# Kernel tuning notes

Hardware: AMD Instinct MI355X
Metric: run time of the kernel (lower is better)

The kernel has to match this reference:

```python
import jax, jax.numpy as jnp
import numpy as np

# NVFP4 E2M1 representable magnitudes and decision midpoints (round-to-nearest)
_E2M1_GRID = np.array([0.0, 0.5, 1.0, 1.5, 2.0, 3.0, 4.0, 6.0], dtype=np.float32)
_E2M1_MIDS = np.array([0.25, 0.75, 1.25, 1.75, 2.5, 3.5, 5.0], dtype=np.float32)
_BLOCK = 16  # quant_tile_shape=(1,16)


def fake_quant_nvfp4(t):
    """Blockwise (16 contiguous elems) E2M1 fake quant with pow2 scales."""
    shape = t.shape
    v = t.reshape(-1, _BLOCK)                      # [n_blocks, 16]
    amax = jnp.max(jnp.abs(v), axis=-1, keepdims=True)
    # power-of-2 scale so that amax/scale <= 6 (E2M1 max)
    exp = jnp.ceil(jnp.log2(jnp.maximum(amax, jnp.float32(1e-30)) / 6.0))
    scale = jnp.where(amax > 0, jnp.exp2(exp), jnp.float32(1.0))
    u = v / scale
    a = jnp.abs(u)
    grid = jnp.asarray(_E2M1_GRID, dtype=t.dtype)
    mids = jnp.asarray(_E2M1_MIDS, dtype=t.dtype)
    idx = jnp.digitize(a, mids)                    # nearest E2M1 magnitude index
    q = jnp.sign(u) * grid[idx]
    return (q * scale).reshape(shape)


def setup_inputs() -> dict:
    key = jax.random.key(0)
    kx, kw = jax.random.split(key)
    x = jax.random.normal(kx, (32, 256, 64, 64), dtype=jnp.float32)
    w = jax.random.normal(kw, (256, 256, 3, 3), dtype=jnp.float32) * 0.05
    return {"x": x, "w": w}


def reference(x, w):
    qx = fake_quant_nvfp4(x)
    qw = fake_quant_nvfp4(w)
    # conv2d, stride 1, padding 1, no bias, NCHW / OIHW
    return jax.lax.conv_general_dilated(
        qx, qw,
        window_strides=(1, 1),
        padding=((1, 1), (1, 1)),
        dimension_numbers=("NCHW", "OIHW", "NCHW"),
    )
```

## Files before the change

kernel.cpp:

```cpp
#include <hip/hip_runtime.h>
#include <stdint.h>
#include <stddef.h>

typedef __attribute__((ext_vector_type(8))) short short8;
typedef __attribute__((ext_vector_type(4))) float f32x4;

#define N_IMG 32
#define C_IN  256
#define HH    64
#define WW    64
#define O_OUT 256
#define HP    66
#define WP    66

#define QX_ELEMS (N_IMG*HP*WP*C_IN)
#define QX_BYTES ((size_t)QX_ELEMS*2)
#define QW_ELEMS (9*O_OUT*C_IN)


__device__ __forceinline__ float e2m1_mag(float a) {
    return a < 0.25f ? 0.0f
         : a < 0.75f ? 0.5f
         : a < 1.25f ? 1.0f
         : a < 1.75f ? 1.5f
         : a < 2.5f  ? 2.0f
         : a < 3.5f  ? 3.0f
         : a < 5.0f  ? 4.0f : 6.0f;
}

__device__ __forceinline__ void blk_scale2(float amax, float& s, float& inv) {
    float ac = fmaxf(amax, 1e-30f);
    int e;
    float m = frexpf(ac, &e);
    int ex = (m > 0.75f) ? (e - 2) : (e - 3);
    if (amax > 0.0f) { s = ldexpf(1.0f, ex); inv = ldexpf(1.0f, -ex); }
    else             { s = 1.0f; inv = 1.0f; }
}

__device__ __forceinline__ unsigned short to_bf16_bits(float v) {
    union { float f; unsigned int u; } cv; cv.f = v;
    return (unsigned short)(cv.u >> 16);
}

__global__ __launch_bounds__(256) void halo_zero_kernel(unsigned short* __restrict__ qx) {
    int id = blockIdx.x * 256 + threadIdx.x;
    size_t off;
    if (id < 135168) {
        int n = id / 4224, r = id % 4224;
        int h = (r / 2112) * 65;
        int k = r % 2112;
        off = (((size_t)(n*HP + h)) * WP) * C_IN + (size_t)k * 8;
    } else {
        int j = id - 135168;
        int n = j >> 12, r = j & 4095;
        int h = 1 + (r >> 6);
        int w = ((r >> 5) & 1) * 65;
        int k = r & 31;
        off = (((size_t)(n*HP + h)) * WP + w) * C_IN + (size_t)k * 8;
    }
    uint4 z; z.x = z.y = z.z = z.w = 0u;
    *(uint4*)(qx + off) = z;
}

__global__ __launch_bounds__(256) void quant_x_kernel(const float* __restrict__ x,
                                                      unsigned short* __restrict__ qx) {
    __shared__ float xf[64][65];
    __shared__ float sarr[4][65];
    __shared__ float iarr[4][65];

    const int bid = blockIdx.x;
    const int n  = bid >> 8;
    const int h  = (bid >> 2) & 63;
    const int cb = bid & 3;
    const int t  = threadIdx.x;

    {
        const int rb = t >> 4;
        const int w4 = (t & 15) * 4;
        const float* src = x + (((size_t)(n*C_IN + cb*64)) * HH + h) * WW;
#pragma unroll
        for (int it = 0; it < 4; ++it) {
            int r = it * 16 + rb;
            float4 g = *(const float4*)(src + (size_t)r * (HH*WW) + w4);
            xf[r][w4+0] = g.x; xf[r][w4+1] = g.y; xf[r][w4+2] = g.z; xf[r][w4+3] = g.w;
        }
    }
    __syncthreads();

    {
        const int c = t >> 2, wb = t & 3;
        float amax = 0.f;
#pragma unroll
        for (int j = 0; j < 16; ++j) amax = fmaxf(amax, fabsf(xf[c][wb*16 + j]));
        float s, inv;
        blk_scale2(amax, s, inv);
        sarr[wb][c] = s;
        iarr[wb][c] = inv;
    }
    __syncthreads();

    {
        const int w = t >> 2, cg = (t & 3) * 16, wb = w >> 4;
        unsigned short outv[16];
#pragma unroll
        for (int i = 0; i < 16; ++i) {
            int c = cg + i;
            float v = xf[c][w];
            float q = copysignf(e2m1_mag(fabsf(v) * iarr[wb][c]) * sarr[wb][c], v);
            outv[i] = to_bf16_bits(q);
        }
        unsigned short* dst = qx + (((size_t)(n*HP + h + 1)) * WP + (w + 1)) * C_IN + cb*64 + cg;
        *(uint4*)(dst)     = *(const uint4*)&outv[0];
        *(uint4*)(dst + 8) = *(const uint4*)&outv[8];
    }
}

__global__ __launch_bounds__(256) void quant_w_kernel(const float* __restrict__ w,
                                                      unsigned short* __restrict__ qw) {
    __shared__ unsigned short lq[2304];
    const int o = blockIdx.x;
    const int t = threadIdx.x;
    const float* src = w + (size_t)o * 2304;
    if (t < 144) {
        float v[16];
#pragma unroll
        for (int j = 0; j < 4; ++j) {
            float4 f = ((const float4*)(src + t*16))[j];
            v[j*4+0]=f.x; v[j*4+1]=f.y; v[j*4+2]=f.z; v[j*4+3]=f.w;
        }
        float amax = 0.f;
#pragma unroll
        for (int j = 0; j < 16; ++j) amax = fmaxf(amax, fabsf(v[j]));
        float s, inv;
        blk_scale2(amax, s, inv);
#pragma unroll
        for (int j = 0; j < 16; ++j)
            lq[t*16 + j] = to_bf16_bits(copysignf(e2m1_mag(fabsf(v[j]) * inv) * s, v[j]));
    }
    __syncthreads();
#pragma unroll
    for (int p = 0; p < 9; ++p)
        qw[((size_t)(p*O_OUT + o)) * C_IN + t] = lq[t*9 + p];
}

__device__ __forceinline__ void gld16(void* lds, const void* g) {
    __builtin_amdgcn_global_load_lds(
        (const __attribute__((address_space(1))) unsigned int*)g,
        (__attribute__((address_space(3))) unsigned int*)lds,
        16, 0, 0);
}

__device__ __forceinline__ short8 rd8(const void* p) {
    return *(const short8*)p;
}

#define MFMA16 __builtin_amdgcn_mfma_f32_16x16x32_bf16

#define MM16(I0, A00, A01, A10, A11)                                      \
    do {                                                                  \
        _Pragma("unroll")                                                 \
        for (int j = 0; j < 4; ++j) {                                     \
            acc[I0][j]     = MFMA16(A00, b[j][0], acc[I0][j],     0,0,0); \
            acc[I0][j]     = MFMA16(A01, b[j][1], acc[I0][j],     0,0,0); \
            acc[(I0)+1][j] = MFMA16(A10, b[j][0], acc[(I0)+1][j], 0,0,0); \
            acc[(I0)+1][j] = MFMA16(A11, b[j][1], acc[(I0)+1][j], 0,0,0); \
        }                                                                 \
    } while (0)

#define PHASE(Q, S1, S2, VM)                                              \
    do {                                                                  \
        short8 aa0 = rd8(LA + rA + (2*(Q))*2048   + cA0);                 \
        short8 aa1 = rd8(LA + rA + (2*(Q))*2048   + (cA0^64));            \
        short8 aa2 = rd8(LA + rA + (2*(Q)+1)*2048 + cA0);                 \
        short8 aa3 = rd8(LA + rA + (2*(Q)+1)*2048 + (cA0^64));            \
        S1; S2;                                                           \
        __builtin_amdgcn_s_barrier();                                     \
        asm volatile("s_waitcnt lgkmcnt(0)" ::: "memory");                \
        __builtin_amdgcn_sched_barrier(0);                                \
        __builtin_amdgcn_s_setprio(1);                                    \
        MM16(2*(Q), aa0, aa1, aa2, aa3);                                  \
        __builtin_amdgcn_s_setprio(0);                                    \
        asm volatile("s_waitcnt " VM ::: "memory");                       \
        __builtin_amdgcn_s_barrier();                                     \
    } while (0)

__global__ __launch_bounds__(512) void conv_kernel(const unsigned short* __restrict__ qw,
                                                   const unsigned short* __restrict__ qx,
                                                   float* __restrict__ out) {
    __shared__ unsigned short lds[65536];
    char* Lc = (char*)lds;

    const int tid  = threadIdx.x;
    const int w    = tid >> 6;
    const int lane = tid & 63;
    const int lo16 = lane & 15;
    const int quad = lane >> 4;
    const int wm   = w & 1;
    const int wn   = w >> 1;

    const int id  = blockIdx.x;
    const int idx = id >> 3;
    const int n   = (id & 7) + ((idx >> 4) << 3);
    const int pt  = idx & 15;
    const int h0  = pt * 4;
    const int hw0 = pt * 256;

    const int trow  = tid >> 3;
    const int c_off = ((tid & 7) ^ (trow & 7)) << 3;
    const unsigned short* gB = qx + ((size_t)((n*HP + h0 + 1) * WP + trow + 1)) * C_IN + c_off;
    const int ro0 = trow + ((tid >= 256) ? 96 : 0);
    const unsigned short* gA = qw + (size_t)ro0 * C_IN + c_off;
    const int awb = w * 1024 + ((w < 4) ? 0 : 12288);
    const int bwb = w * 1024;

    const int key = (lo16 & 7) << 4;
    const int cA0 = (quad << 4) ^ key;
    const int rA  = (wm * 128 + lo16) * 128;
    const int rB  = (wn * 64  + lo16) * 128;

    f32x4 acc[8][4];
#pragma unroll
    for (int i = 0; i < 8; ++i)
#pragma unroll
        for (int j = 0; j < 4; ++j)
            acc[i][j] = (f32x4){0.f, 0.f, 0.f, 0.f};

    {
        const unsigned short* ga = gA;
        const unsigned short* gb = gB - 17152;
        char* SA = Lc;
        char* SB = Lc + 32768;
        gld16(SB + bwb,         gb);
        gld16(SB + bwb + 8192,  gb + 16896);
        gld16(SB + bwb + 16384, gb + 2*16896);
        gld16(SB + bwb + 24576, gb + 3*16896);
        gld16(SA + awb,         ga);
        gld16(SA + awb + 4096,  ga + 8192);
        gld16(SA + awb + 8192,  ga + 16384);
        gld16(SA + awb + 12288, ga + 24576);
        asm volatile("s_waitcnt vmcnt(0)" ::: "memory");
        __builtin_amdgcn_s_barrier();
    }

    int curOff = 0;
#pragma unroll 1
    for (int t = 0; t < 36; ++t) {
        const int tn  = (t < 35) ? (t + 1) : 35;
        const int pn  = tn >> 2;
        const int qn  = pn / 3;
        const int dwn = pn - qn * 3;
        const int cn  = (tn & 3) << 6;
        const unsigned short* ga = gA + pn * 65536 + cn;
        const unsigned short* gb = gB + (ptrdiff_t)((qn - 1) * WP + (dwn - 1)) * C_IN + cn;

        const char* LA = Lc + curOff;
        const char* LB = LA + 32768;
        char* SA = Lc + (curOff ^ 65536);
        char* SB = SA + 32768;

        short8 b[4][2];
#pragma unroll
        for (int j = 0; j < 4; ++j) {
            b[j][0] = rd8(LB + rB + j*2048 + cA0);
            b[j][1] = rd8(LB + rB + j*2048 + (cA0^64));
        }

        PHASE(0, gld16(SB + bwb,         gb),
                 gld16(SB + bwb + 8192,  gb + 16896),   "vmcnt(4)");
        PHASE(1, gld16(SB + bwb + 16384, gb + 2*16896),
                 gld16(SB + bwb + 24576, gb + 3*16896), "vmcnt(5)");
        PHASE(2, gld16(SA + awb,         ga),
                 gld16(SA + awb + 4096,  ga + 8192),    "vmcnt(6)");
        PHASE(3, gld16(SA + awb + 8192,  ga + 16384),
                 gld16(SA + awb + 12288, ga + 24576),   "vmcnt(3)");

        curOff ^= 65536;
    }

#pragma unroll
    for (int i = 0; i < 8; ++i) {
        const int o = wm * 128 + i * 16 + quad * 4;
        float* orow = out + ((size_t)(n * O_OUT + o)) * (HH*WW) + hw0 + wn * 64 + lo16;
#pragma unroll
        for (int j = 0; j < 4; ++j) {
            float* dst = orow + j * 16;
#pragma unroll
            for (int r = 0; r < 4; ++r)
                dst[(size_t)r * (HH*WW)] = acc[i][j][r];
        }
    }
}

extern "C" void kernel_launch(void* const* d_in, const int* in_sizes, int n_in,
                              void* d_out, int out_size, void* d_ws, size_t ws_size,
                              hipStream_t stream) {
    const float* x = (const float*)d_in[0];
    const float* w = (const float*)d_in[1];
    float* out = (float*)d_out;

    unsigned short* qx = (unsigned short*)d_ws;
    unsigned short* qw = (unsigned short*)((char*)d_ws + QX_BYTES);

    halo_zero_kernel<<<dim3(1040), 256, 0, stream>>>(qx);
    quant_x_kernel<<<dim3(N_IMG*HH*4), 256, 0, stream>>>(x, qx);
    quant_w_kernel<<<dim3(O_OUT), 256, 0, stream>>>(w, qw);
    conv_kernel<<<dim3(512), 512, 0, stream>>>(qw, qx, out);
}
```

Baseline: 363.3 us.

## Software-pipeline LDS fragment reads one phase ahead of MFMA in conv main loop

Restructures the main loop so each phase issues the LDS reads for the next A-fragment group before running the current MFMAs. The B fragments for the next tile are read during the last phase, using ping-pong registers. The loop is unrolled by two to alternate buffers, and the vmcnt wait counts are adjusted to match. This hides LDS read latency behind matrix work, at the cost of more live registers (roughly double the A/B fragment registers) and tighter waitcnt correctness requirements.

```diff
diff --git a/kernel.cpp b/kernel.cpp
--- a/kernel.cpp
+++ b/kernel.cpp
@@ -156,32 +156,81 @@
 
 #define MFMA16 __builtin_amdgcn_mfma_f32_16x16x32_bf16
 
-#define MM16(I0, A00, A01, A10, A11)                                      \
+#define MM16(I0, A00, A01, A10, A11, B)                                   \
     do {                                                                  \
         _Pragma("unroll")                                                 \
         for (int j = 0; j < 4; ++j) {                                     \
-            acc[I0][j]     = MFMA16(A00, b[j][0], acc[I0][j],     0,0,0); \
-            acc[I0][j]     = MFMA16(A01, b[j][1], acc[I0][j],     0,0,0); \
-            acc[(I0)+1][j] = MFMA16(A10, b[j][0], acc[(I0)+1][j], 0,0,0); \
-            acc[(I0)+1][j] = MFMA16(A11, b[j][1], acc[(I0)+1][j], 0,0,0); \
+            acc[I0][j]     = MFMA16(A00, B[j][0], acc[I0][j],     0,0,0); \
+            acc[I0][j]     = MFMA16(A01, B[j][1], acc[I0][j],     0,0,0); \
+            acc[(I0)+1][j] = MFMA16(A10, B[j][0], acc[(I0)+1][j], 0,0,0); \
+            acc[(I0)+1][j] = MFMA16(A11, B[j][1], acc[(I0)+1][j], 0,0,0); \
         }                                                                 \
     } while (0)
 
-#define PHASE(Q, S1, S2, VM)                                              \
+#define RDQ(D0, D1, D2, D3, Q)                                            \
+    D0 = rd8(LA + rA + (2*(Q))*2048   + cA0);                             \
+    D1 = rd8(LA + rA + (2*(Q))*2048   + (cA0^64));                        \
+    D2 = rd8(LA + rA + (2*(Q)+1)*2048 + cA0);                             \
+    D3 = rd8(LA + rA + (2*(Q)+1)*2048 + (cA0^64));
+
+#define PH_OPEN()                                                         \
+    __builtin_amdgcn_s_barrier();                                         \
+    asm volatile("s_waitcnt lgkmcnt(0)" ::: "memory");                    \
+    __builtin_amdgcn_sched_barrier(0);                                    \
+    __builtin_amdgcn_s_setprio(1);
+
+#define PH_CLOSE(VM)                                                      \
+    __builtin_amdgcn_s_setprio(0);                                        \
+    asm volatile("s_waitcnt " VM ::: "memory");                           \
+    __builtin_amdgcn_s_barrier();
+
+#define CONV_TILE(TN, LAOFF, BCUR, BNXT)                                  \
     do {                                                                  \
-        short8 aa0 = rd8(LA + rA + (2*(Q))*2048   + cA0);                 \
-        short8 aa1 = rd8(LA + rA + (2*(Q))*2048   + (cA0^64));            \
-        short8 aa2 = rd8(LA + rA + (2*(Q)+1)*2048 + cA0);                 \
-        short8 aa3 = rd8(LA + rA + (2*(Q)+1)*2048 + (cA0^64));            \
-        S1; S2;                                                           \
-        __builtin_amdgcn_s_barrier();                                     \
-        asm volatile("s_waitcnt lgkmcnt(0)" ::: "memory");                \
-        __builtin_amdgcn_sched_barrier(0);                                \
-        __builtin_amdgcn_s_setprio(1);                                    \
-        MM16(2*(Q), aa0, aa1, aa2, aa3);                                  \
-        __builtin_amdgcn_s_setprio(0);                                    \
-        asm volatile("s_waitcnt " VM ::: "memory");                       \
-        __builtin_amdgcn_s_barrier();                                     \
+        const int tn  = (TN);                                             \
+        const int pn  = tn >> 2;                                          \
+        const int qn  = pn / 3;                                           \
+        const int dwn = pn - qn * 3;                                      \
+        const int cn  = (tn & 3) << 6;                                    \
+        const unsigned short* ga = gA + pn * 65536 + cn;                  \
+        const unsigned short* gb = gB + (ptrdiff_t)((qn - 1) * WP + (dwn - 1)) * C_IN + cn; \
+        const char* LA = Lc + (LAOFF);                                    \
+        char* SA = Lc + ((LAOFF) ^ 65536);                                \
+        char* SB = SA + 32768;                                            \
+        short8 aA0, aA1, aA2, aA3, aB0, aB1, aB2, aB3;                    \
+        \
+        RDQ(aA0, aA1, aA2, aA3, 0);                                       \
+                     \
+        gld16(SB + bwb,        gb);                                       \
+        gld16(SB + bwb + 8192, gb + 16896);                               \
+        PH_OPEN();                                                        \
+        RDQ(aB0, aB1, aB2, aB3, 1);                                       \
+        MM16(0, aA0, aA1, aA2, aA3, BCUR);                                \
+        PH_CLOSE("vmcnt(3)");                                             \
+                            \
+        gld16(SB + bwb + 16384, gb + 2*16896);                            \
+        gld16(SB + bwb + 24576, gb + 3*16896);                            \
+        PH_OPEN();                                                        \
+        RDQ(aA0, aA1, aA2, aA3, 2);                                       \
+        MM16(2, aB0, aB1, aB2, aB3, BCUR);                                \
+        PH_CLOSE("vmcnt(4)");                                             \
+                            \
+        gld16(SA + awb,        ga);                                       \
+        gld16(SA + awb + 4096, ga + 8192);                                \
+        PH_OPEN();                                                        \
+        RDQ(aB0, aB1, aB2, aB3, 3);                                       \
+        MM16(4, aA0, aA1, aA2, aA3, BCUR);                                \
+        PH_CLOSE("vmcnt(2)");                                             \
+          \
+        gld16(SA + awb + 8192,  ga + 16384);                              \
+        gld16(SA + awb + 12288, ga + 24576);                              \
+        PH_OPEN();                                                        \
+        _Pragma("unroll")                                                 \
+        for (int j = 0; j < 4; ++j) {                                     \
+            BNXT[j][0] = rd8(SB + rB + j*2048 + cA0);                     \
+            BNXT[j][1] = rd8(SB + rB + j*2048 + (cA0^64));                \
+        }                                                                 \
+        MM16(6, aB0, aB1, aB2, aB3, BCUR);                                \
+        PH_CLOSE("vmcnt(2)");                                             \
     } while (0)
 
 __global__ __launch_bounds__(512) void conv_kernel(const unsigned short* __restrict__ qw,
@@ -242,40 +291,24 @@
         __builtin_amdgcn_s_barrier();
     }
 
-    int curOff = 0;
+    short8 b0[4][2], b1[4][2];
+    {
+        const char* LB = Lc + 32768;
+#pragma unroll
+        for (int j = 0; j < 4; ++j) {
+            b0[j][0] = rd8(LB + rB + j*2048 + cA0);
+            b0[j][1] = rd8(LB + rB + j*2048 + (cA0^64));
+        }
+    }
+
 #pragma unroll 1
-    for (int t = 0; t < 36; ++t) {
-        const int tn  = (t < 35) ? (t + 1) : 35;
-        const int pn  = tn >> 2;
-        const int qn  = pn / 3;
-        const int dwn = pn - qn * 3;
-        const int cn  = (tn & 3) << 6;
-        const unsigned short* ga = gA + pn * 65536 + cn;
-        const unsigned short* gb = gB + (ptrdiff_t)((qn - 1) * WP + (dwn - 1)) * C_IN + cn;
-
-        const char* LA = Lc + curOff;
-        const char* LB = LA + 32768;
-        char* SA = Lc + (curOff ^ 65536);
-        char* SB = SA + 32768;
-
-        short8 b[4][2];
-#pragma unroll
-        for (int j = 0; j < 4; ++j) {
-            b[j][0] = rd8(LB + rB + j*2048 + cA0);
-            b[j][1] = rd8(LB + rB + j*2048 + (cA0^64));
-        }
-
-        PHASE(0, gld16(SB + bwb,         gb),
-                 gld16(SB + bwb + 8192,  gb + 16896),   "vmcnt(4)");
-        PHASE(1, gld16(SB + bwb + 16384, gb + 2*16896),
-                 gld16(SB + bwb + 24576, gb + 3*16896), "vmcnt(5)");
-        PHASE(2, gld16(SA + awb,         ga),
-                 gld16(SA + awb + 4096,  ga + 8192),    "vmcnt(6)");
-        PHASE(3, gld16(SA + awb + 8192,  ga + 16384),
-                 gld16(SA + awb + 12288, ga + 24576),   "vmcnt(3)");
-
-        curOff ^= 65536;
-    }
+    for (int tt = 0; tt < 18; ++tt) {
+        const int t0 = tt * 2;
+        CONV_TILE(t0 + 1, 0, b0, b1);
+        CONV_TILE((t0 + 2 < 36) ? (t0 + 2) : 35, 65536, b1, b0);
+    }
+
+    asm volatile("s_waitcnt vmcnt(0)" ::: "memory");
 
 #pragma unroll
     for (int i = 0; i < 8; ++i) {
```

After: 350.1 us. 1.04x faster.
